# Optimization experiments

Hardware: AMD Instinct MI355X
Metric: run time of the kernel (lower is better)

The kernel has to match this reference:

```python
import jax, jax.numpy as jnp
import numpy as np

H = 16  # hidden size (hardwired in the module)


def setup_inputs() -> dict:
    key = jax.random.key(0)
    ks = jax.random.split(key, 7)
    B, S, C, P = 512, 336, 321, 96
    s = 1.0 / np.sqrt(H)
    x = jax.random.normal(ks[0], (B, S, C), dtype=jnp.float32)
    W_ih = jax.random.uniform(ks[1], (4 * H, 1), jnp.float32, -s, s)
    W_hh = jax.random.uniform(ks[2], (4 * H, H), jnp.float32, -s, s)
    b_ih = jax.random.uniform(ks[3], (4 * H,), jnp.float32, -s, s)
    b_hh = jax.random.uniform(ks[4], (4 * H,), jnp.float32, -s, s)
    W_fc = jax.random.uniform(ks[5], (P, H), jnp.float32, -s, s)
    b_fc = jax.random.uniform(ks[6], (P,), jnp.float32, -s, s)
    return {"x": x, "W_ih": W_ih, "W_hh": W_hh, "b_ih": b_ih,
            "b_hh": b_hh, "W_fc": W_fc, "b_fc": b_fc}


def reference(x, W_ih, W_hh, b_ih, b_hh, W_fc, b_fc):
    B, S, C = x.shape
    N = B * C  # fused batch of independent univariate sequences
    # [B,S,C] -> [B,C,S] -> [N,S,1] -> time-major [S,N,1]
    xs = jnp.transpose(x, (0, 2, 1)).reshape(N, S, 1)
    xs = jnp.transpose(xs, (1, 0, 2))
    # precompute input projection + both biases for all timesteps: [S,N,4H]
    x_proj = xs @ W_ih.T + (b_ih + b_hh)

    def step(carry, xp):
        h, c = carry
        pre = xp + h @ W_hh.T  # [N,4H], PyTorch gate order i,f,g,o
        i = jax.nn.sigmoid(pre[:, 0 * H:1 * H])
        f = jax.nn.sigmoid(pre[:, 1 * H:2 * H])
        g = jnp.tanh(pre[:, 2 * H:3 * H])
        o = jax.nn.sigmoid(pre[:, 3 * H:4 * H])
        c = f * c + i * g
        h = o * jnp.tanh(c)
        return (h, c), None

    h0 = jnp.zeros((N, H), x.dtype)
    (h_last, _), _ = jax.lax.scan(step, (h0, h0), x_proj)
    pred = h_last @ W_fc.T + b_fc  # [N, P]
    pred = pred.reshape(B, C, -1)
    return jnp.transpose(pred, (0, 2, 1))  # [B, P, C]
```

## Files before the change

kernel.cpp:

```cpp
#include <hip/hip_runtime.h>
#include <stdint.h>


typedef _Float16 half8 __attribute__((ext_vector_type(8)));
typedef float floatx4 __attribute__((ext_vector_type(4)));

#define HH 16
#define SS 336
#define CCD 321
#define BBD 512
#define PPD 96
#define NSEQ (BBD * CCD)
#define NTILES (NSEQ / 16)

#define TABN 1024
#define SIG_SCALE 64.0f
#define TANH_SCALE 128.0f
#define IDX_OFF 512.0f
#define IDX_MAX 1022.995f

static_assert(NSEQ % 16 == 0, "tile exactness");
static_assert(NTILES % 4 == 0, "block exactness");

union U32H2 { uint32_t u; _Float16 h[2]; };
union BFrag { uint32_t u[4]; half8 v; };

__device__ __forceinline__ float lut(const float2* __restrict__ tab, float y) {
    y = __builtin_amdgcn_fmed3f(y, 0.0f, IDX_MAX);
    float fr = __builtin_amdgcn_fractf(y);
    int i = (int)y;
    float2 e = tab[i];
    return fmaf(fr, e.y, e.x);
}

__global__ __launch_bounds__(256) void lstm_fused(
    const float* __restrict__ x,
    const float* __restrict__ W_ih,
    const float* __restrict__ W_hh,
    const float* __restrict__ b_ih,
    const float* __restrict__ b_hh,
    const float* __restrict__ W_fc,
    const float* __restrict__ b_fc,
    float* __restrict__ out)
{
    __shared__ float2 sig_tab[TABN];
    __shared__ float2 tanh_tab[TABN];

    for (int i = (int)threadIdx.x; i < TABN; i += 256) {
        float x0 = ((float)i       - IDX_OFF) / SIG_SCALE;
        float x1 = ((float)(i + 1) - IDX_OFF) / SIG_SCALE;
        float s0 = 1.0f / (1.0f + expf(-x0));
        float s1 = 1.0f / (1.0f + expf(-x1));
        sig_tab[i] = make_float2(s0, s1 - s0);
        float u0 = ((float)i       - IDX_OFF) / TANH_SCALE;
        float u1 = ((float)(i + 1) - IDX_OFF) / TANH_SCALE;
        float t0 = tanhf(u0);
        float t1 = tanhf(u1);
        tanh_tab[i] = make_float2(t0, t1 - t0);
    }
    __syncthreads();

    const int lane = (int)(threadIdx.x & 63u);
    const int wid  = (int)(threadIdx.x >> 6u);
    const int tile = (int)blockIdx.x * 4 + wid;
    if (tile >= NTILES) return;

    const int n16 = lane & 15;
    const int g   = lane >> 4;

    const int n = tile * 16 + n16;
    const int b = n / CCD;
    const int c = n - b * CCD;

    const float gate_scale[4] = { SIG_SCALE, SIG_SCALE, TANH_SCALE, SIG_SCALE };

    half8 a_frag[4];
    #pragma unroll
    for (int t = 0; t < 4; ++t) {
        const int j = t * 16 + n16;
        const float sc = gate_scale[t];
        #pragma unroll
        for (int i = 0; i < 8; ++i) {
            const int k = g * 8 + i;
            float w = 0.0f;
            if (k < 16)       w = W_hh[j * 16 + k];
            else if (k == 16) w = W_ih[j];
            a_frag[t][i] = (_Float16)(w * sc);
        }
    }
    floatx4 bias_frag[4];
    #pragma unroll
    for (int t = 0; t < 4; ++t) {
        #pragma unroll
        for (int r = 0; r < 4; ++r) {
            const int j = t * 16 + g * 4 + r;
            bias_frag[t][r] = (b_ih[j] + b_hh[j]) * gate_scale[t] + IDX_OFF;
        }
    }

    const int selA = n16 + ((g << 5) & 63);
    const int selB = selA + 16;

    uint32_t hv0 = 0u, hv1 = 0u;
    float cst[4] = {0.f, 0.f, 0.f, 0.f};

    const float* xptr = x + (size_t)b * (SS * CCD) + c;
    float xcur = xptr[0];

    for (int s = 0; s < SS; ++s) {
        float xnext = (s + 1 < SS) ? xptr[(s + 1) * CCD] : 0.0f;

        uint32_t s0 = (uint32_t)__shfl((int)hv0, selA, 64);
        uint32_t s1 = (uint32_t)__shfl((int)hv1, selA, 64);
        uint32_t s2 = (uint32_t)__shfl((int)hv0, selB, 64);
        uint32_t s3 = (uint32_t)__shfl((int)hv1, selB, 64);

        U32H2 xp; xp.h[0] = (_Float16)xcur; xp.h[1] = (_Float16)0.0f;

        BFrag bf;
        bf.u[0] = (g < 2) ? s0 : ((g == 2) ? xp.u : 0u);
        bf.u[1] = (g < 2) ? s1 : 0u;
        bf.u[2] = (g < 2) ? s2 : 0u;
        bf.u[3] = (g < 2) ? s3 : 0u;

        floatx4 ai = __builtin_amdgcn_mfma_f32_16x16x32_f16(a_frag[0], bf.v, bias_frag[0], 0, 0, 0);
        floatx4 af = __builtin_amdgcn_mfma_f32_16x16x32_f16(a_frag[1], bf.v, bias_frag[1], 0, 0, 0);
        floatx4 ag = __builtin_amdgcn_mfma_f32_16x16x32_f16(a_frag[2], bf.v, bias_frag[2], 0, 0, 0);
        floatx4 ao = __builtin_amdgcn_mfma_f32_16x16x32_f16(a_frag[3], bf.v, bias_frag[3], 0, 0, 0);

        float hn[4];
        #pragma unroll
        for (int r = 0; r < 4; ++r) {
            float iv = lut(sig_tab,  ai[r]);
            float fv = lut(sig_tab,  af[r]);
            float gv = lut(tanh_tab, ag[r]);
            float ov = lut(sig_tab,  ao[r]);
            float cc = fmaf(fv, cst[r], iv * gv);
            cst[r] = cc;
            float tc = lut(tanh_tab, fmaf(cc, TANH_SCALE, IDX_OFF));
            hn[r] = ov * tc;
        }

        U32H2 p0, p1;
        p0.h[0] = (_Float16)hn[0]; p0.h[1] = (_Float16)hn[1];
        p1.h[0] = (_Float16)hn[2]; p1.h[1] = (_Float16)hn[3];
        hv0 = p0.u; hv1 = p1.u;
        xcur = xnext;
    }

    uint32_t s0 = (uint32_t)__shfl((int)hv0, selA, 64);
    uint32_t s1 = (uint32_t)__shfl((int)hv1, selA, 64);
    uint32_t s2 = (uint32_t)__shfl((int)hv0, selB, 64);
    uint32_t s3 = (uint32_t)__shfl((int)hv1, selB, 64);

    BFrag bfc;
    bfc.u[0] = (g < 2) ? s0 : 0u;
    bfc.u[1] = (g < 2) ? s1 : 0u;
    bfc.u[2] = (g < 2) ? s2 : 0u;
    bfc.u[3] = (g < 2) ? s3 : 0u;

    const size_t obase = (size_t)b * (PPD * CCD) + c;
    #pragma unroll
    for (int t = 0; t < 6; ++t) {
        half8 afc;
        #pragma unroll
        for (int i = 0; i < 8; ++i) {
            const int k = g * 8 + i;
            float w = (k < 16) ? W_fc[(t * 16 + n16) * 16 + k] : 0.0f;
            afc[i] = (_Float16)w;
        }
        floatx4 cf;
        #pragma unroll
        for (int r = 0; r < 4; ++r) cf[r] = b_fc[t * 16 + g * 4 + r];

        floatx4 d = __builtin_amdgcn_mfma_f32_16x16x32_f16(afc, bfc.v, cf, 0, 0, 0);

        #pragma unroll
        for (int r = 0; r < 4; ++r) {
            const int p = t * 16 + g * 4 + r;
            out[obase + (size_t)p * CCD] = d[r];
        }
    }
}

extern "C" void kernel_launch(void* const* d_in, const int* in_sizes, int n_in,
                              void* d_out, int out_size, void* d_ws, size_t ws_size,
                              hipStream_t stream) {
    const float* x    = (const float*)d_in[0];
    const float* W_ih = (const float*)d_in[1];
    const float* W_hh = (const float*)d_in[2];
    const float* b_ih = (const float*)d_in[3];
    const float* b_hh = (const float*)d_in[4];
    const float* W_fc = (const float*)d_in[5];
    const float* b_fc = (const float*)d_in[6];
    float* out = (float*)d_out;

    dim3 grid(NTILES / 4);
    dim3 block(256);
    hipLaunchKernelGGL(lstm_fused, grid, block, 0, stream,
                       x, W_ih, W_hh, b_ih, b_hh, W_fc, b_fc, out);
}
```

Baseline: 1.190 ms.

## Process two independent sequence tiles per wavefront to interleave recurrences

Each wavefront now carries two independent 16-sequence tiles through the time loop. It issues their MFMAs and table lookups back to back, so one tile's latency chain can overlap with the other's. This targets the serial dependency latency of the recurrence, since a single tile per wave leaves the MFMA and LDS pipes idle. In exchange the grid is halved, which lowers the number of waves available to hide latency across the GPU, and register use per thread goes up.

```diff
diff --git a/kernel.cpp b/kernel.cpp
--- a/kernel.cpp
+++ b/kernel.cpp
@@ -12,6 +12,7 @@
 #define PPD 96
 #define NSEQ (BBD * CCD)
 #define NTILES (NSEQ / 16)
+#define TPW 2
 
 #define TABN 1024
 #define SIG_SCALE 64.0f
@@ -20,7 +21,7 @@
 #define IDX_MAX 1022.995f
 
 static_assert(NSEQ % 16 == 0, "tile exactness");
-static_assert(NTILES % 4 == 0, "block exactness");
+static_assert(NTILES % (4 * TPW) == 0, "block exactness");
 
 union U32H2 { uint32_t u; _Float16 h[2]; };
 union BFrag { uint32_t u[4]; half8 v; };
@@ -62,15 +63,10 @@
 
     const int lane = (int)(threadIdx.x & 63u);
     const int wid  = (int)(threadIdx.x >> 6u);
-    const int tile = (int)blockIdx.x * 4 + wid;
-    if (tile >= NTILES) return;
+    const int tile0 = ((int)blockIdx.x * 4 + wid) * TPW;
 
     const int n16 = lane & 15;
     const int g   = lane >> 4;
-
-    const int n = tile * 16 + n16;
-    const int b = n / CCD;
-    const int c = n - b * CCD;
 
     const float gate_scale[4] = { SIG_SCALE, SIG_SCALE, TANH_SCALE, SIG_SCALE };
 
@@ -101,65 +97,86 @@
     const int selA = n16 + ((g << 5) & 63);
     const int selB = selA + 16;
 
-    uint32_t hv0 = 0u, hv1 = 0u;
-    float cst[4] = {0.f, 0.f, 0.f, 0.f};
-
-    const float* xptr = x + (size_t)b * (SS * CCD) + c;
-    float xcur = xptr[0];
+    uint32_t hv0[TPW], hv1[TPW];
+    float cst[TPW][4];
+    const float* xptr[TPW];
+    float xcur[TPW];
+    #pragma unroll
+    for (int tt = 0; tt < TPW; ++tt) {
+        hv0[tt] = 0u; hv1[tt] = 0u;
+        #pragma unroll
+        for (int r = 0; r < 4; ++r) cst[tt][r] = 0.0f;
+        const int n = (tile0 + tt) * 16 + n16;
+        const int b = n / CCD;
+        const int c = n - b * CCD;
+        xptr[tt] = x + (size_t)b * (SS * CCD) + c;
+        xcur[tt] = xptr[tt][0];
+    }
 
     for (int s = 0; s < SS; ++s) {
-        float xnext = (s + 1 < SS) ? xptr[(s + 1) * CCD] : 0.0f;
-
-        uint32_t s0 = (uint32_t)__shfl((int)hv0, selA, 64);
-        uint32_t s1 = (uint32_t)__shfl((int)hv1, selA, 64);
-        uint32_t s2 = (uint32_t)__shfl((int)hv0, selB, 64);
-        uint32_t s3 = (uint32_t)__shfl((int)hv1, selB, 64);
-
-        U32H2 xp; xp.h[0] = (_Float16)xcur; xp.h[1] = (_Float16)0.0f;
-
-        BFrag bf;
-        bf.u[0] = (g < 2) ? s0 : ((g == 2) ? xp.u : 0u);
-        bf.u[1] = (g < 2) ? s1 : 0u;
-        bf.u[2] = (g < 2) ? s2 : 0u;
-        bf.u[3] = (g < 2) ? s3 : 0u;
-
-        floatx4 ai = __builtin_amdgcn_mfma_f32_16x16x32_f16(a_frag[0], bf.v, bias_frag[0], 0, 0, 0);
-        floatx4 af = __builtin_amdgcn_mfma_f32_16x16x32_f16(a_frag[1], bf.v, bias_frag[1], 0, 0, 0);
-        floatx4 ag = __builtin_amdgcn_mfma_f32_16x16x32_f16(a_frag[2], bf.v, bias_frag[2], 0, 0, 0);
-        floatx4 ao = __builtin_amdgcn_mfma_f32_16x16x32_f16(a_frag[3], bf.v, bias_frag[3], 0, 0, 0);
-
-        float hn[4];
-        #pragma unroll
-        for (int r = 0; r < 4; ++r) {
-            float iv = lut(sig_tab,  ai[r]);
-            float fv = lut(sig_tab,  af[r]);
-            float gv = lut(tanh_tab, ag[r]);
-            float ov = lut(sig_tab,  ao[r]);
-            float cc = fmaf(fv, cst[r], iv * gv);
-            cst[r] = cc;
-            float tc = lut(tanh_tab, fmaf(cc, TANH_SCALE, IDX_OFF));
-            hn[r] = ov * tc;
-        }
-
-        U32H2 p0, p1;
-        p0.h[0] = (_Float16)hn[0]; p0.h[1] = (_Float16)hn[1];
-        p1.h[0] = (_Float16)hn[2]; p1.h[1] = (_Float16)hn[3];
-        hv0 = p0.u; hv1 = p1.u;
-        xcur = xnext;
-    }
-
-    uint32_t s0 = (uint32_t)__shfl((int)hv0, selA, 64);
-    uint32_t s1 = (uint32_t)__shfl((int)hv1, selA, 64);
-    uint32_t s2 = (uint32_t)__shfl((int)hv0, selB, 64);
-    uint32_t s3 = (uint32_t)__shfl((int)hv1, selB, 64);
-
-    BFrag bfc;
-    bfc.u[0] = (g < 2) ? s0 : 0u;
-    bfc.u[1] = (g < 2) ? s1 : 0u;
-    bfc.u[2] = (g < 2) ? s2 : 0u;
-    bfc.u[3] = (g < 2) ? s3 : 0u;
-
-    const size_t obase = (size_t)b * (PPD * CCD) + c;
+        float xnext[TPW];
+        #pragma unroll
+        for (int tt = 0; tt < TPW; ++tt)
+            xnext[tt] = (s + 1 < SS) ? xptr[tt][(s + 1) * CCD] : 0.0f;
+
+        BFrag bf[TPW];
+        #pragma unroll
+        for (int tt = 0; tt < TPW; ++tt) {
+            uint32_t s0 = (uint32_t)__shfl((int)hv0[tt], selA, 64);
+            uint32_t s1 = (uint32_t)__shfl((int)hv1[tt], selA, 64);
+            uint32_t s2 = (uint32_t)__shfl((int)hv0[tt], selB, 64);
+            uint32_t s3 = (uint32_t)__shfl((int)hv1[tt], selB, 64);
+            U32H2 xp; xp.h[0] = (_Float16)xcur[tt]; xp.h[1] = (_Float16)0.0f;
+            bf[tt].u[0] = (g < 2) ? s0 : ((g == 2) ? xp.u : 0u);
+            bf[tt].u[1] = (g < 2) ? s1 : 0u;
+            bf[tt].u[2] = (g < 2) ? s2 : 0u;
+            bf[tt].u[3] = (g < 2) ? s3 : 0u;
+        }
+
+        floatx4 acc[TPW][4];
+        #pragma unroll
+        for (int t = 0; t < 4; ++t) {
+            #pragma unroll
+            for (int tt = 0; tt < TPW; ++tt)
+                acc[tt][t] = __builtin_amdgcn_mfma_f32_16x16x32_f16(
+                    a_frag[t], bf[tt].v, bias_frag[t], 0, 0, 0);
+        }
+
+        #pragma unroll
+        for (int tt = 0; tt < TPW; ++tt) {
+            float hn[4];
+            #pragma unroll
+            for (int r = 0; r < 4; ++r) {
+                float iv = lut(sig_tab,  acc[tt][0][r]);
+                float fv = lut(sig_tab,  acc[tt][1][r]);
+                float gv = lut(tanh_tab, acc[tt][2][r]);
+                float ov = lut(sig_tab,  acc[tt][3][r]);
+                float cc = fmaf(fv, cst[tt][r], iv * gv);
+                cst[tt][r] = cc;
+                float tc = lut(tanh_tab, fmaf(cc, TANH_SCALE, IDX_OFF));
+                hn[r] = ov * tc;
+            }
+            U32H2 p0, p1;
+            p0.h[0] = (_Float16)hn[0]; p0.h[1] = (_Float16)hn[1];
+            p1.h[0] = (_Float16)hn[2]; p1.h[1] = (_Float16)hn[3];
+            hv0[tt] = p0.u; hv1[tt] = p1.u;
+            xcur[tt] = xnext[tt];
+        }
+    }
+
+    BFrag bfc[TPW];
+    #pragma unroll
+    for (int tt = 0; tt < TPW; ++tt) {
+        uint32_t s0 = (uint32_t)__shfl((int)hv0[tt], selA, 64);
+        uint32_t s1 = (uint32_t)__shfl((int)hv1[tt], selA, 64);
+        uint32_t s2 = (uint32_t)__shfl((int)hv0[tt], selB, 64);
+        uint32_t s3 = (uint32_t)__shfl((int)hv1[tt], selB, 64);
+        bfc[tt].u[0] = (g < 2) ? s0 : 0u;
+        bfc[tt].u[1] = (g < 2) ? s1 : 0u;
+        bfc[tt].u[2] = (g < 2) ? s2 : 0u;
+        bfc[tt].u[3] = (g < 2) ? s3 : 0u;
+    }
+
     #pragma unroll
     for (int t = 0; t < 6; ++t) {
         half8 afc;
@@ -173,12 +190,18 @@
         #pragma unroll
         for (int r = 0; r < 4; ++r) cf[r] = b_fc[t * 16 + g * 4 + r];
 
-        floatx4 d = __builtin_amdgcn_mfma_f32_16x16x32_f16(afc, bfc.v, cf, 0, 0, 0);
-
-        #pragma unroll
-        for (int r = 0; r < 4; ++r) {
-            const int p = t * 16 + g * 4 + r;
-            out[obase + (size_t)p * CCD] = d[r];
+        #pragma unroll
+        for (int tt = 0; tt < TPW; ++tt) {
+            floatx4 d = __builtin_amdgcn_mfma_f32_16x16x32_f16(afc, bfc[tt].v, cf, 0, 0, 0);
+            const int n = (tile0 + tt) * 16 + n16;
+            const int b = n / CCD;
+            const int c = n - b * CCD;
+            const size_t obase = (size_t)b * (PPD * CCD) + c;
+            #pragma unroll
+            for (int r = 0; r < 4; ++r) {
+                const int p = t * 16 + g * 4 + r;
+                out[obase + (size_t)p * CCD] = d[r];
+            }
         }
     }
 }
@@ -195,7 +218,7 @@
     const float* b_fc = (const float*)d_in[6];
     float* out = (float*)d_out;
 
-    dim3 grid(NTILES / 4);
+    dim3 grid(NTILES / (4 * TPW));
     dim3 block(256);
     hipLaunchKernelGGL(lstm_fused, grid, block, 0, stream,
                        x, W_ih, W_hh, b_ih, b_hh, W_fc, b_fc, out);
```

After: 1.359 ms. +14.2%, slower.
